# Kernel tuning notes

Measured on AMD Instinct MI355X. Metric: run time of the kernel, lower is better.

Reference implementation:

```python
import jax, jax.numpy as jnp
import numpy as np
import math

D_MODEL, D_INNER, D_STATE, D_CONV, DT_RANK = 768, 1536, 16, 4, 48
BATCH, SEQLEN = 2, 1024
DT_MIN, DT_MAX = 1e-4, 1.0


def setup_inputs() -> dict:
    key = jax.random.key(0)
    ks = jax.random.split(key, 10)
    D, N, R, K = D_INNER, D_STATE, DT_RANK, D_CONV
    total_out = 2 * D + R + 2 * D * N

    def xavier(k, shape):
        fan_in, fan_out = shape[1], shape[0]
        a = math.sqrt(6.0 / (fan_in + fan_out))
        return jax.random.uniform(k, shape, jnp.float32, -a, a)

    x = jax.random.normal(ks[0], (BATCH, SEQLEN, D_MODEL), jnp.float32)
    W_in = xavier(ks[1], (total_out, D_MODEL))
    W_dt = xavier(ks[2], (D, R))
    W_out = xavier(ks[3], (D_MODEL, D))
    W_res = xavier(ks[4], (D, D_MODEL))
    conv_w = jax.random.normal(ks[5], (D, K), jnp.float32) * (1.0 / math.sqrt(K))
    conv_b = jnp.zeros((D,), jnp.float32)
    # A_log init: log(1..N) per inner channel
    A_log = jnp.broadcast_to(jnp.log(jnp.arange(1, N + 1, dtype=jnp.float32)), (D, N))
    Dskip = jnp.ones((D,), jnp.float32)
    # dt_bias = inverse_softplus(exp(uniform in [log dt_min, log dt_max]))
    dt = jnp.exp(jax.random.uniform(ks[6], (D,), jnp.float32) * (math.log(DT_MAX) - math.log(DT_MIN)) + math.log(DT_MIN))
    dt_bias = dt + jnp.log(-jnp.expm1(-dt))
    norm_w = jnp.ones((D,), jnp.float32)
    ln_w = jnp.ones((D_MODEL,), jnp.float32)
    ln_b = jnp.zeros((D_MODEL,), jnp.float32)
    return {
        "x": x, "ln_w": ln_w, "ln_b": ln_b, "W_in": W_in, "W_dt": W_dt,
        "conv_w": conv_w, "conv_b": conv_b, "A_log": A_log, "Dskip": Dskip,
        "dt_bias": dt_bias, "norm_w": norm_w, "W_res": W_res, "W_out": W_out,
    }


def _forward(x, ln_w, ln_b, W_in, W_dt, conv_w, conv_b, A_log, Dskip, dt_bias, norm_w, W_res, W_out):
    B, L, _ = x.shape
    D, N = A_log.shape
    K = conv_w.shape[1]
    R = W_dt.shape[1]
    # pre LayerNorm
    mu = x.mean(-1, keepdims=True)
    var = ((x - mu) ** 2).mean(-1, keepdims=True)
    xn = (x - mu) * jax.lax.rsqrt(var + 1e-5) * ln_w + ln_b
    # fused input projection, then split
    p = jnp.einsum('bld,od->blo', xn, W_in)  # (B,L,2D+R+2DN)
    z = p[..., :D]
    u = p[..., D:2 * D]
    dth = p[..., 2 * D:2 * D + R]
    Bpar = p[..., 2 * D + R:2 * D + R + D * N].reshape(B, L, D, N)
    Cpar = p[..., 2 * D + R + D * N:].reshape(B, L, D, N)
    # causal depthwise conv over time on u
    uc = jax.lax.conv_general_dilated(
        u.transpose(0, 2, 1), conv_w[:, None, :], (1,), [(K - 1, 0)],
        feature_group_count=D, dimension_numbers=('NCH', 'OIH', 'NCH'))
    u = (uc + conv_b[None, :, None]).transpose(0, 2, 1)  # (B,L,D)
    # dt: low-rank proj + bias -> softplus -> clamp
    dt = jnp.clip(jax.nn.softplus(jnp.einsum('blr,dr->bld', dth, W_dt) + dt_bias), DT_MIN, DT_MAX)
    A = -jnp.exp(A_log)  # (D,N), negative
    dA = jnp.exp(dt[..., None] * A)          # (B,L,D,N)
    dBu = (dt * u)[..., None] * Bpar         # (B,L,D,N)

    def step(h, inp):
        dA_t, dBu_t, C_t = inp               # each (B,D,N)
        h = dA_t * h + dBu_t
        return h, (C_t * h).sum(-1)          # y_t: (B,D)

    h0 = jnp.zeros((B, D, N), x.dtype)
    _, ys = jax.lax.scan(step, h0, (dA.transpose(1, 0, 2, 3),
                                    dBu.transpose(1, 0, 2, 3),
                                    Cpar.transpose(1, 0, 2, 3)))
    y = ys.transpose(1, 0, 2) + u * Dskip    # (B,L,D)
    # fused gated RMSNorm + inner residual
    res = jnp.einsum('blm,dm->bld', x, W_res)
    g = y * jax.nn.silu(z)
    g = g * jax.lax.rsqrt((g * g).mean(-1, keepdims=True) + 1e-6) * norm_w + res
    return jnp.einsum('bld,md->blm', g, W_out)


def reference(x, ln_w, ln_b, W_in, W_dt, conv_w, conv_b, A_log, Dskip, dt_bias, norm_w, W_res, W_out):
    return _forward(x, ln_w, ln_b, W_in, W_dt, conv_w, conv_b, A_log, Dskip, dt_bias, norm_w, W_res, W_out)
```

## Files before the change

### kernel.cpp

```cpp
#include <hip/hip_runtime.h>


typedef unsigned short u16;
typedef __bf16 bf16x8 __attribute__((ext_vector_type(8)));
typedef float f32x4 __attribute__((ext_vector_type(4)));

#define OPAD 52480
#define OTOT 52272
#define DI   1536
#define DM   768
#define Z0   0
#define U0   1536
#define DTH0 3072
#define B0   3120
#define C0   27696

#define SCAN_P 64
#define SCAN_T 16
#define SPF    4

__device__ static inline u16 f2bf(float f) {
    unsigned u = __float_as_uint(f);
    u += 0x7fffu + ((u >> 16) & 1u);
    return (u16)(u >> 16);
}
__device__ static inline float bf2f(u16 s) {
    return __uint_as_float(((unsigned)s) << 16);
}

__device__ static inline void gload16(const void* g, void* l) {
    __builtin_amdgcn_global_load_lds(
        (const __attribute__((address_space(1))) unsigned int*)g,
        (__attribute__((address_space(3))) unsigned int*)l, 16, 0, 0);
}

__device__ static inline void unpack8(uint4 v, float* f) {
    unsigned w0 = v.x, w1 = v.y, w2 = v.z, w3 = v.w;
    f[0] = __uint_as_float(w0 << 16); f[1] = __uint_as_float(w0 & 0xffff0000u);
    f[2] = __uint_as_float(w1 << 16); f[3] = __uint_as_float(w1 & 0xffff0000u);
    f[4] = __uint_as_float(w2 << 16); f[5] = __uint_as_float(w2 & 0xffff0000u);
    f[6] = __uint_as_float(w3 << 16); f[7] = __uint_as_float(w3 & 0xffff0000u);
}

__global__ void cvt_kernel(const float* __restrict__ src, u16* __restrict__ dst,
                           long n_src, long n_tot) {
    long i4 = ((long)blockIdx.x * 256 + threadIdx.x) * 4;
    if (i4 >= n_tot) return;
    ushort4 o;
    if (i4 < n_src) {
        float4 v = *(const float4*)(src + i4);
        o.x = f2bf(v.x); o.y = f2bf(v.y); o.z = f2bf(v.z); o.w = f2bf(v.w);
    } else {
        o.x = o.y = o.z = o.w = 0;
    }
    *(ushort4*)(dst + i4) = o;
}

__device__ static inline void block_reduce2(float& a, float& b) {
    #pragma unroll
    for (int o = 32; o > 0; o >>= 1) {
        a += __shfl_down(a, o);
        b += __shfl_down(b, o);
    }
    __shared__ float sa[4], sb[4];
    int lane = threadIdx.x & 63, w = threadIdx.x >> 6;
    if (lane == 0) { sa[w] = a; sb[w] = b; }
    __syncthreads();
    a = sa[0] + sa[1] + sa[2] + sa[3];
    b = sb[0] + sb[1] + sb[2] + sb[3];
}

__global__ void __launch_bounds__(256) ln_kernel(const float* __restrict__ x,
        const float* __restrict__ w, const float* __restrict__ b,
        u16* __restrict__ xnbf, u16* __restrict__ xbf) {
    int m = blockIdx.x, tid = threadIdx.x;
    const float* xr = x + (size_t)m * DM;
    float v[3];
    v[0] = xr[tid]; v[1] = xr[tid + 256]; v[2] = xr[tid + 512];
    float s = v[0] + v[1] + v[2];
    float ss = v[0]*v[0] + v[1]*v[1] + v[2]*v[2];
    block_reduce2(s, ss);
    float mu = s * (1.f / DM);
    float var = ss * (1.f / DM) - mu * mu;
    float inv = rsqrtf(var + 1e-5f);
    #pragma unroll
    for (int i = 0; i < 3; ++i) {
        int d = tid + i * 256;
        float xn = (v[i] - mu) * inv * w[d] + b[d];
        xnbf[(size_t)m * DM + d] = f2bf(xn);
        xbf[(size_t)m * DM + d] = f2bf(v[i]);
    }
}

template <int OUT_BF16>
__global__ void __launch_bounds__(256) gemm_bt(const u16* __restrict__ A,
        const u16* __restrict__ B, void* __restrict__ C, int K, int ldc) {
    __shared__ u16 smem[2 * 128 * 64];
    u16* As = smem;
    u16* Bs = smem + 128 * 64;
    int tid = threadIdx.x;
    int m0 = blockIdx.x * 128, n0 = blockIdx.y * 128;
    int lane = tid & 63, wave = tid >> 6;
    int wm = wave >> 1, wn = wave & 1;
    int l15 = lane & 15, l4 = lane >> 4;
    f32x4 acc[4][4] = {};
    const u16* Ag = A + (size_t)m0 * K;
    const u16* Bg = B + (size_t)n0 * K;
    int crow = tid >> 3;
    int ccol = ((tid & 7) ^ ((tid >> 3) & 7)) * 8;
    int ldsoff = (tid & 192) * 16;
    int xr = l15 & 7;

    for (int k0 = 0; k0 < K; k0 += 64) {
        __syncthreads();
        #pragma unroll
        for (int it = 0; it < 4; ++it) {
            gload16(Ag + (size_t)(it * 32 + crow) * K + k0 + ccol,
                    (char*)As + it * 4096 + ldsoff);
            gload16(Bg + (size_t)(it * 32 + crow) * K + k0 + ccol,
                    (char*)Bs + it * 4096 + ldsoff);
        }
        __syncthreads();
        const u16* Arow = As + (wm * 64 + l15) * 64;
        const u16* Brow = Bs + (wn * 64 + l15) * 64;
        #pragma unroll
        for (int kk8 = 0; kk8 < 8; kk8 += 4) {
            int sw = ((l4 + kk8) ^ xr) * 8;
            bf16x8 af[4], bfr[4];
            #pragma unroll
            for (int i = 0; i < 4; ++i) af[i] = *(const bf16x8*)(Arow + i * 16 * 64 + sw);
            #pragma unroll
            for (int j = 0; j < 4; ++j) bfr[j] = *(const bf16x8*)(Brow + j * 16 * 64 + sw);
            #pragma unroll
            for (int i = 0; i < 4; ++i)
                #pragma unroll
                for (int j = 0; j < 4; ++j)
                    acc[i][j] = __builtin_amdgcn_mfma_f32_16x16x32_bf16(
                        af[i], bfr[j], acc[i][j], 0, 0, 0);
        }
    }
    #pragma unroll
    for (int i = 0; i < 4; ++i) {
        int row = m0 + wm * 64 + i * 16 + l4 * 4;
        #pragma unroll
        for (int j = 0; j < 4; ++j) {
            int col = n0 + wn * 64 + j * 16 + l15;
            #pragma unroll
            for (int r = 0; r < 4; ++r) {
                size_t off = (size_t)(row + r) * ldc + col;
                if (OUT_BF16) ((u16*)C)[off] = f2bf(acc[i][j][r]);
                else          ((float*)C)[off] = acc[i][j][r];
            }
        }
    }
}

#define G2_BUF  65536
#define G2_HALF 16384
#define G2_BOFF 32768

__global__ void __launch_bounds__(512, 2) gemm256_bt(const u16* __restrict__ A,
        const u16* __restrict__ B, u16* __restrict__ C, int K, int ldc) {
    __shared__ u16 smem[65536];
    char* smemc = (char*)smem;
    const int tid = threadIdx.x;
    const int l = tid & 63, w = tid >> 6;
    const int wm = w >> 2, wn = w & 3;
    const int l15 = l & 15, l4 = l >> 4;
    const int flat = blockIdx.y * 8 + blockIdx.x;
    const int wg = (flat & 7) * 205 + (flat >> 3);
    const int m0 = (wg & 7) * 256, n0 = (wg >> 3) * 256;
    const int NT = K >> 6;

    const int rA = l15 >> 1;
    const int rdoff = rA * 128 + ((((l4 << 1) + (l15 & 1)) ^ ((rA & 3) << 1)) << 4);
    const int wpr = (l & 7) ^ (((l >> 3) & 3) << 1);
    const int srow = w * 32 + ((l >> 3) << 1) + (wpr & 1);
    const u16* Ast = A + (size_t)(m0 + srow) * K + (wpr >> 1) * 8;
    const u16* Bst = B + (size_t)(n0 + srow) * K + (wpr >> 1) * 8;
    const int sdst = w * 2048;

    f32x4 acc[8][4] = {};
    bf16x8 bvK[4];

#define G2_STAGE(MATP, MOFF, nxt, sh, tk)                                      \
    gload16(MATP + (size_t)(tk) * 64 + (sh) * 32,                              \
            smemc + (nxt) * G2_BUF + (MOFF) + (sh) * G2_HALF + sdst);          \
    gload16(MATP + (size_t)16 * K + (size_t)(tk) * 64 + (sh) * 32,             \
            smemc + (nxt) * G2_BUF + (MOFF) + (sh) * G2_HALF + sdst + 1024);

#define G2_PHASE(cur, nxt, rh, h, READB, SMAT, SMOFF, sh, tk, DO_VM)           \
    {                                                                          \
        G2_STAGE(SMAT, SMOFF, nxt, sh, tk);                                    \
        const char* Ab = smemc + (cur) * G2_BUF + (h) * G2_HALF                \
                         + (wm * 128 + (rh) * 64) * 64 + rdoff;                \
        bf16x8 af[4];                                                          \
        if (READB) {                                                           \
            const char* Bb = smemc + (cur) * G2_BUF + G2_BOFF + (h) * G2_HALF  \
                             + (wn * 64) * 64 + rdoff;                         \
            _Pragma("unroll")                                                  \
            for (int j = 0; j < 4; ++j)                                        \
                bvK[j] = *(const bf16x8*)(Bb + j * 1024);                      \
        }                                                                      \
        _Pragma("unroll")                                                      \
        for (int i = 0; i < 4; ++i) af[i] = *(const bf16x8*)(Ab + i * 1024);   \
        __builtin_amdgcn_s_barrier();                                          \
        __builtin_amdgcn_s_setprio(1);                                         \
        _Pragma("unroll")                                                      \
        for (int i = 0; i < 4; ++i)                                            \
            _Pragma("unroll")                                                  \
            for (int j = 0; j < 4; ++j)                                        \
                acc[(rh) * 4 + i][j] = __builtin_amdgcn_mfma_f32_16x16x32_bf16(\
                    af[i], bvK[j], acc[(rh) * 4 + i][j], 0, 0, 0);             \
        __builtin_amdgcn_s_setprio(0);                                         \
        if (DO_VM) asm volatile("s_waitcnt vmcnt(4)" ::: "memory");            \
        __builtin_amdgcn_s_barrier();                                          \
    }

#define G2_TILE(cur, nxt, tk)                                                  \
    G2_PHASE(cur, nxt, 0, 0, 1, Ast, 0,       0, tk, 0)                        \
    G2_PHASE(cur, nxt, 1, 0, 0, Bst, G2_BOFF, 0, tk, 1)                        \
    G2_PHASE(cur, nxt, 0, 1, 1, Ast, 0,       1, tk, 0)                        \
    G2_PHASE(cur, nxt, 1, 1, 0, Bst, G2_BOFF, 1, tk, 1)

    G2_STAGE(Ast, 0,       0, 0, 0);
    G2_STAGE(Bst, G2_BOFF, 0, 0, 0);
    G2_STAGE(Ast, 0,       0, 1, 0);
    G2_STAGE(Bst, G2_BOFF, 0, 1, 0);
    asm volatile("s_waitcnt vmcnt(4)" ::: "memory");
    __builtin_amdgcn_s_barrier();

    for (int t = 0; t < NT; t += 2) {
        int tk1 = t + 1;
        int tk2 = (t + 2 < NT) ? t + 2 : NT - 1;
        G2_TILE(0, 1, tk1)
        G2_TILE(1, 0, tk2)
    }

    #pragma unroll
    for (int ai = 0; ai < 8; ++ai) {
        int row = m0 + wm * 128 + ai * 16 + l4 * 4;
        #pragma unroll
        for (int j = 0; j < 4; ++j) {
            int col = n0 + wn * 64 + j * 16 + l15;
            #pragma unroll
            for (int r = 0; r < 4; ++r)
                C[(size_t)(row + r) * ldc + col] = f2bf(acc[ai][j][r]);
        }
    }
#undef G2_STAGE
#undef G2_PHASE
#undef G2_TILE
}

__global__ void __launch_bounds__(256) conv_kernel(const u16* __restrict__ p,
        const float* __restrict__ cw, const float* __restrict__ cb,
        float* __restrict__ u) {
    int d = blockIdx.x * 256 + threadIdx.x;
    int m = blockIdx.y;
    int l = m & 1023;
    int bm = m - l;
    float acc = cb[d];
    #pragma unroll
    for (int j = 0; j < 4; ++j) {
        int ls = l - 3 + j;
        if (ls >= 0)
            acc += cw[d * 4 + j] * bf2f(p[(size_t)(bm + ls) * OPAD + U0 + d]);
    }
    u[(size_t)m * DI + d] = acc;
}

__global__ void __launch_bounds__(256) dt_kernel(const u16* __restrict__ p,
        const float* __restrict__ Wdt, const float* __restrict__ dt_bias,
        float* __restrict__ dt) {
    int m0 = blockIdx.x * 16, tid = threadIdx.x;
    __shared__ float dth_s[16 * 48];
    for (int i = tid; i < 16 * 48; i += 256)
        dth_s[i] = bf2f(p[(size_t)(m0 + i / 48) * OPAD + DTH0 + (i % 48)]);
    __syncthreads();
    #pragma unroll
    for (int ii = 0; ii < 6; ++ii) {
        int d = ii * 256 + tid;
        float base = dt_bias[d];
        float acc[16];
        #pragma unroll
        for (int mm = 0; mm < 16; ++mm) acc[mm] = base;
        for (int r = 0; r < 48; ++r) {
            float wv = Wdt[d * 48 + r];
            #pragma unroll
            for (int mm = 0; mm < 16; ++mm)
                acc[mm] = fmaf(wv, dth_s[mm * 48 + r], acc[mm]);
        }
        #pragma unroll
        for (int mm = 0; mm < 16; ++mm) {
            float xv = acc[mm];
            float sp = xv > 20.f ? xv : log1pf(__expf(xv));
            sp = fminf(fmaxf(sp, 1e-4f), 1.0f);
            dt[(size_t)(m0 + mm) * DI + d] = sp;
        }
    }
}

__global__ void __launch_bounds__(256, 2) scan1_kernel(const u16* __restrict__ p,
        const float* __restrict__ dt, const float* __restrict__ u,
        const float* __restrict__ A_log,
        float* __restrict__ chkA, float* __restrict__ chkB) {
    int d = blockIdx.x * 256 + threadIdx.x;
    int b = blockIdx.y, c = blockIdx.z;
    int t0base = c * SCAN_T;
    float a[16];
    #pragma unroll
    for (int n = 0; n < 16; ++n) a[n] = -__expf(A_log[d * 16 + n]);
    const u16* pB = p + (size_t)(b * 1024 + t0base) * OPAD + B0 + d * 16;
    const float* dtp = dt + (size_t)(b * 1024 + t0base) * DI + d;
    const float* up  = u  + (size_t)(b * 1024 + t0base) * DI + d;
    uint4 Br[SPF][2]; float dtr[SPF], ur[SPF];
    #pragma unroll
    for (int i = 0; i < SPF; ++i) {
        Br[i][0] = *(const uint4*)(pB + (size_t)i * OPAD);
        Br[i][1] = *(const uint4*)(pB + (size_t)i * OPAD + 8);
        dtr[i] = dtp[(size_t)i * DI];
        ur[i]  = up[(size_t)i * DI];
    }
    float h[16], Av[16];
    #pragma unroll
    for (int n = 0; n < 16; ++n) { h[n] = 0.f; Av[n] = 1.f; }
    for (int t0 = 0; t0 < SCAN_T; t0 += SPF) {
        #pragma unroll
        for (int s = 0; s < SPF; ++s) {
            int t = t0 + s;
            uint4 b0 = Br[s][0], b1 = Br[s][1];
            float dtv = dtr[s], uv = ur[s];
            int tl = t + SPF < SCAN_T ? t + SPF : SCAN_T - 1;
            Br[s][0] = *(const uint4*)(pB + (size_t)tl * OPAD);
            Br[s][1] = *(const uint4*)(pB + (size_t)tl * OPAD + 8);
            dtr[s] = dtp[(size_t)tl * DI];
            ur[s]  = up[(size_t)tl * DI];
            float Bf[16];
            unpack8(b0, Bf); unpack8(b1, Bf + 8);
            float dtu = dtv * uv;
            #pragma unroll
            for (int n = 0; n < 16; ++n) {
                float dA = __expf(dtv * a[n]);
                h[n] = fmaf(dA, h[n], dtu * Bf[n]);
                Av[n] *= dA;
            }
        }
    }
    size_t o = (((size_t)c * 2 + b) * 1536 + d) * 16;
    #pragma unroll
    for (int k = 0; k < 4; ++k) {
        *(float4*)(chkA + o + k * 4) = make_float4(Av[4*k], Av[4*k+1], Av[4*k+2], Av[4*k+3]);
        *(float4*)(chkB + o + k * 4) = make_float4(h[4*k], h[4*k+1], h[4*k+2], h[4*k+3]);
    }
}

__global__ void __launch_bounds__(256) scan_comb_kernel(const float* __restrict__ chkA,
        const float* __restrict__ chkB, float* __restrict__ hstart) {
    int idx = blockIdx.x * 256 + threadIdx.x;
    float hs = 0.f;
    for (int c = 0; c < SCAN_P; ++c) {
        size_t o = (size_t)c * 49152 + idx;
        hstart[o] = hs;
        hs = fmaf(chkA[o], hs, chkB[o]);
    }
}

__global__ void __launch_bounds__(256, 2) scan2_kernel(const u16* __restrict__ p,
        const float* __restrict__ dt, const float* __restrict__ u,
        const float* __restrict__ A_log, const float* __restrict__ Dskip,
        const float* __restrict__ hstart, float* __restrict__ y) {
    int d = blockIdx.x * 256 + threadIdx.x;
    int b = blockIdx.y, c = blockIdx.z;
    int t0base = c * SCAN_T;
    float a[16];
    #pragma unroll
    for (int n = 0; n < 16; ++n) a[n] = -__expf(A_log[d * 16 + n]);
    float Dsk = Dskip[d];
    const u16* pB = p + (size_t)(b * 1024 + t0base) * OPAD + B0 + d * 16;
    const u16* pC = p + (size_t)(b * 1024 + t0base) * OPAD + C0 + d * 16;
    const float* dtp = dt + (size_t)(b * 1024 + t0base) * DI + d;
    const float* up  = u  + (size_t)(b * 1024 + t0base) * DI + d;
    float* yp        = y  + (size_t)(b * 1024 + t0base) * DI + d;
    uint4 Br[SPF][2], Cr[SPF][2]; float dtr[SPF], ur[SPF];
    #pragma unroll
    for (int i = 0; i < SPF; ++i) {
        Br[i][0] = *(const uint4*)(pB + (size_t)i * OPAD);
        Br[i][1] = *(const uint4*)(pB + (size_t)i * OPAD + 8);
        Cr[i][0] = *(const uint4*)(pC + (size_t)i * OPAD);
        Cr[i][1] = *(const uint4*)(pC + (size_t)i * OPAD + 8);
        dtr[i] = dtp[(size_t)i * DI];
        ur[i]  = up[(size_t)i * DI];
    }
    float h[16];
    {
        size_t o = ((size_t)c * 3072 + (size_t)b * 1536 + d) * 16;
        #pragma unroll
        for (int k = 0; k < 4; ++k) {
            float4 hv = *(const float4*)(hstart + o + k * 4);
            h[4*k] = hv.x; h[4*k+1] = hv.y; h[4*k+2] = hv.z; h[4*k+3] = hv.w;
        }
    }
    for (int t0 = 0; t0 < SCAN_T; t0 += SPF) {
        #pragma unroll
        for (int s = 0; s < SPF; ++s) {
            int t = t0 + s;
            uint4 b0 = Br[s][0], b1 = Br[s][1], c0 = Cr[s][0], c1 = Cr[s][1];
            float dtv = dtr[s], uv = ur[s];
            int tl = t + SPF < SCAN_T ? t + SPF : SCAN_T - 1;
            Br[s][0] = *(const uint4*)(pB + (size_t)tl * OPAD);
            Br[s][1] = *(const uint4*)(pB + (size_t)tl * OPAD + 8);
            Cr[s][0] = *(const uint4*)(pC + (size_t)tl * OPAD);
            Cr[s][1] = *(const uint4*)(pC + (size_t)tl * OPAD + 8);
            dtr[s] = dtp[(size_t)tl * DI];
            ur[s]  = up[(size_t)tl * DI];
            float Bf[16], Cf[16];
            unpack8(b0, Bf); unpack8(b1, Bf + 8);
            unpack8(c0, Cf); unpack8(c1, Cf + 8);
            float dtu = dtv * uv;
            #pragma unroll
            for (int n = 0; n < 16; ++n) {
                float dA = __expf(dtv * a[n]);
                h[n] = fmaf(dA, h[n], dtu * Bf[n]);
            }
            float a0 = fmaf(Cf[0], h[0], uv * Dsk), a1 = Cf[1] * h[1];
            float a2 = Cf[2] * h[2], a3 = Cf[3] * h[3];
            #pragma unroll
            for (int n = 4; n < 16; n += 4) {
                a0 = fmaf(Cf[n],   h[n],   a0);
                a1 = fmaf(Cf[n+1], h[n+1], a1);
                a2 = fmaf(Cf[n+2], h[n+2], a2);
                a3 = fmaf(Cf[n+3], h[n+3], a3);
            }
            yp[(size_t)t * DI] = (a0 + a1) + (a2 + a3);
        }
    }
}

__global__ void __launch_bounds__(256) gate_kernel(const u16* __restrict__ p,
        const float* __restrict__ y, const float* __restrict__ res,
        const float* __restrict__ norm_w, u16* __restrict__ g) {
    int m = blockIdx.x, tid = threadIdx.x;
    const u16* pz = p + (size_t)m * OPAD + Z0;
    const float* yr = y + (size_t)m * DI;
    float gp[6];
    float ss = 0.f, dummy = 0.f;
    #pragma unroll
    for (int i = 0; i < 6; ++i) {
        int d = i * 256 + tid;
        float z = bf2f(pz[d]);
        float gv = yr[d] * z / (1.f + __expf(-z));
        gp[i] = gv;
        ss += gv * gv;
    }
    block_reduce2(ss, dummy);
    float scale = rsqrtf(ss * (1.f / DI) + 1e-6f);
    #pragma unroll
    for (int i = 0; i < 6; ++i) {
        int d = i * 256 + tid;
        float val = gp[i] * scale * norm_w[d] + res[(size_t)m * DI + d];
        g[(size_t)m * DI + d] = f2bf(val);
    }
}

extern "C" void kernel_launch(void* const* d_in, const int* in_sizes, int n_in,
                              void* d_out, int out_size, void* d_ws, size_t ws_size,
                              hipStream_t stream) {
    const float* x       = (const float*)d_in[0];
    const float* ln_w    = (const float*)d_in[1];
    const float* ln_b    = (const float*)d_in[2];
    const float* W_in    = (const float*)d_in[3];
    const float* W_dt    = (const float*)d_in[4];
    const float* conv_w  = (const float*)d_in[5];
    const float* conv_b  = (const float*)d_in[6];
    const float* A_log   = (const float*)d_in[7];
    const float* Dskip   = (const float*)d_in[8];
    const float* dt_bias = (const float*)d_in[9];
    const float* norm_w  = (const float*)d_in[10];
    const float* W_res   = (const float*)d_in[11];
    const float* W_out   = (const float*)d_in[12];
    float* out = (float*)d_out;

    char* wsb = (char*)d_ws;
    u16* Wbf     = (u16*)(wsb + 0);
    u16* Wresbf  = (u16*)(wsb + 80609280);
    u16* Woutbf  = (u16*)(wsb + 82968576);
    u16* xnbf    = (u16*)(wsb + 85327872);
    u16* xbf     = (u16*)(wsb + 88473600);
    u16* pbuf    = (u16*)(wsb + 91619328);
    float* ucv   = (float*)(wsb + 306577408);
    float* dtv   = (float*)(wsb + 319160320);
    float* ybuf  = (float*)(wsb + 331743232);
    float* resb  = (float*)(wsb + 344326144);
    u16* gbuf    = (u16*)(wsb + 356909056);
    float* chkA  = (float*)(wsb + 0);
    float* chkB  = (float*)(wsb + 12582912);
    float* hst   = (float*)(wsb + 25165824);

    cvt_kernel<<<39360, 256, 0, stream>>>(W_in, Wbf, (long)OTOT * DM, (long)OPAD * DM);
    cvt_kernel<<<1152, 256, 0, stream>>>(W_res, Wresbf, (long)DI * DM, (long)DI * DM);
    cvt_kernel<<<1152, 256, 0, stream>>>(W_out, Woutbf, (long)DM * DI, (long)DM * DI);
    ln_kernel<<<2048, 256, 0, stream>>>(x, ln_w, ln_b, xnbf, xbf);
    gemm256_bt<<<dim3(8, 205), 512, 0, stream>>>(xnbf, Wbf, pbuf, DM, OPAD);
    gemm_bt<0><<<dim3(16, 12), 256, 0, stream>>>(xbf, Wresbf, resb, DM, DI);
    conv_kernel<<<dim3(6, 2048), 256, 0, stream>>>(pbuf, conv_w, conv_b, ucv);
    dt_kernel<<<128, 256, 0, stream>>>(pbuf, W_dt, dt_bias, dtv);
    scan1_kernel<<<dim3(6, 2, SCAN_P), 256, 0, stream>>>(pbuf, dtv, ucv, A_log, chkA, chkB);
    scan_comb_kernel<<<192, 256, 0, stream>>>(chkA, chkB, hst);
    scan2_kernel<<<dim3(6, 2, SCAN_P), 256, 0, stream>>>(pbuf, dtv, ucv, A_log, Dskip, hst, ybuf);
    gate_kernel<<<2048, 256, 0, stream>>>(pbuf, ybuf, resb, norm_w, gbuf);
    gemm_bt<0><<<dim3(16, 6), 256, 0, stream>>>(gbuf, Woutbf, out, DI, DM);
}
```

Measured before the change: 705.4 us.

## Fuse W_in bf16 conversion into GEMM loads and conv into scan kernels

The big input-projection GEMM now streams the fp32 W_in directly into an LDS scratch area, converts it to bf16 in-kernel (zeroing padded rows), and writes it into the B tile. This removes the separate cvt pass over the ~40M-element weight and its bf16 write and re-read. The depthwise causal conv is also folded into both scan kernels via a rolling 3-value window, which removes the conv kernel and the fp32 u buffer round trip. The cost is double the B-operand global traffic in fp32, extra LDS and more waitcnt/barrier steps in the GEMM pipeline, and duplicated conv arithmetic in scan1 and scan2.

After: 893.8 us. 26.7% more time.

```diff
diff --git a/kernel.cpp b/kernel.cpp
--- a/kernel.cpp
+++ b/kernel.cpp
@@ -26,6 +26,9 @@
 }
 __device__ static inline float bf2f(u16 s) {
     return __uint_as_float(((unsigned)s) << 16);
+}
+__device__ static inline unsigned pack2(float lo, float hi) {
+    return (unsigned)f2bf(lo) | ((unsigned)f2bf(hi) << 16);
 }
 
 __device__ static inline void gload16(const void* g, void* l) {
@@ -158,10 +161,11 @@
 #define G2_BUF  65536
 #define G2_HALF 16384
 #define G2_BOFF 32768
+#define G2_SCR  131072
 
 __global__ void __launch_bounds__(512, 2) gemm256_bt(const u16* __restrict__ A,
-        const u16* __restrict__ B, u16* __restrict__ C, int K, int ldc) {
-    __shared__ u16 smem[65536];
+        const float* __restrict__ B, u16* __restrict__ C, int K, int ldc) {
+    __shared__ u16 smem[81920];
     char* smemc = (char*)smem;
     const int tid = threadIdx.x;
     const int l = tid & 63, w = tid >> 6;
@@ -177,65 +181,94 @@
     const int wpr = (l & 7) ^ (((l >> 3) & 3) << 1);
     const int srow = w * 32 + ((l >> 3) << 1) + (wpr & 1);
     const u16* Ast = A + (size_t)(m0 + srow) * K + (wpr >> 1) * 8;
-    const u16* Bst = B + (size_t)(n0 + srow) * K + (wpr >> 1) * 8;
+    const int nrow0 = n0 + srow, nrow1 = nrow0 + 16;
+    const int oobA = nrow0 >= OTOT, oobB = nrow1 >= OTOT;
+    const float* Bf0 = B + (size_t)(oobA ? 0 : nrow0) * K + (wpr >> 1) * 8;
+    const float* Bf1 = B + (size_t)(oobB ? 0 : nrow1) * K + (wpr >> 1) * 8;
     const int sdst = w * 2048;
 
     f32x4 acc[8][4] = {};
     bf16x8 bvK[4];
 
-#define G2_STAGE(MATP, MOFF, nxt, sh, tk)                                      \
-    gload16(MATP + (size_t)(tk) * 64 + (sh) * 32,                              \
-            smemc + (nxt) * G2_BUF + (MOFF) + (sh) * G2_HALF + sdst);          \
-    gload16(MATP + (size_t)16 * K + (size_t)(tk) * 64 + (sh) * 32,             \
-            smemc + (nxt) * G2_BUF + (MOFF) + (sh) * G2_HALF + sdst + 1024);
-
-#define G2_PHASE(cur, nxt, rh, h, READB, SMAT, SMOFF, sh, tk, DO_VM)           \
+#define G2_ASTAGE(nxt, sh, tk)                                                 \
+    gload16(Ast + (size_t)(tk) * 64 + (sh) * 32,                               \
+            smemc + (nxt) * G2_BUF + (sh) * G2_HALF + sdst);                   \
+    gload16(Ast + (size_t)16 * K + (size_t)(tk) * 64 + (sh) * 32,              \
+            smemc + (nxt) * G2_BUF + (sh) * G2_HALF + sdst + 1024);
+
+#define G2_BISSUE(QS, qh, qc, tk)                                              \
+    {   const float* bq = ((qc) ? Bf1 : Bf0) + (size_t)(tk) * 64 + (qh) * 32;  \
+        gload16(bq,     smemc + G2_SCR + (QS) * 16384 + sdst);                 \
+        gload16(bq + 4, smemc + G2_SCR + (QS) * 16384 + sdst + 1024); }
+
+#define G2_BCVT(QS, wbuf, wh, wc)                                              \
+    {   const char* scr = smemc + G2_SCR + (QS) * 16384 + sdst + l * 16;       \
+        f32x4 flo = *(const f32x4*)scr;                                        \
+        f32x4 fhi = *(const f32x4*)(scr + 1024);                               \
+        uint4 ov;                                                              \
+        ov.x = pack2(flo[0], flo[1]); ov.y = pack2(flo[2], flo[3]);            \
+        ov.z = pack2(fhi[0], fhi[1]); ov.w = pack2(fhi[2], fhi[3]);            \
+        if ((wc) ? oobB : oobA) ov = make_uint4(0, 0, 0, 0);                   \
+        *(uint4*)(smemc + (wbuf) * G2_BUF + G2_BOFF + (wh) * G2_HALF           \
+                  + sdst + (wc) * 1024 + l * 16) = ov; }
+
+#define G2_PH(cur, nxt, rh, h, ASTG, QS, qh, qc, tk, DOW, wbuf, wh, wc, VN)    \
     {                                                                          \
-        G2_STAGE(SMAT, SMOFF, nxt, sh, tk);                                    \
+        asm volatile("s_waitcnt vmcnt(" #VN ")" ::: "memory");                 \
+        if (DOW) { G2_BCVT(QS, wbuf, wh, wc) }                                 \
+        if (ASTG) { G2_ASTAGE(nxt, h, tk) }                                    \
+        G2_BISSUE(QS, qh, qc, tk)                                              \
         const char* Ab = smemc + (cur) * G2_BUF + (h) * G2_HALF                \
                          + (wm * 128 + (rh) * 64) * 64 + rdoff;                \
         bf16x8 af[4];                                                          \
-        if (READB) {                                                           \
+        if (!(rh)) {                                                           \
             const char* Bb = smemc + (cur) * G2_BUF + G2_BOFF + (h) * G2_HALF  \
                              + (wn * 64) * 64 + rdoff;                         \
-            _Pragma("unroll")                                                  \
-            for (int j = 0; j < 4; ++j)                                        \
+            _Pragma("unroll") for (int j = 0; j < 4; ++j)                      \
                 bvK[j] = *(const bf16x8*)(Bb + j * 1024);                      \
         }                                                                      \
-        _Pragma("unroll")                                                      \
-        for (int i = 0; i < 4; ++i) af[i] = *(const bf16x8*)(Ab + i * 1024);   \
+        _Pragma("unroll") for (int i = 0; i < 4; ++i)                          \
+            af[i] = *(const bf16x8*)(Ab + i * 1024);                           \
+        asm volatile("s_waitcnt lgkmcnt(0)" ::: "memory");                     \
         __builtin_amdgcn_s_barrier();                                          \
         __builtin_amdgcn_s_setprio(1);                                         \
-        _Pragma("unroll")                                                      \
-        for (int i = 0; i < 4; ++i)                                            \
-            _Pragma("unroll")                                                  \
-            for (int j = 0; j < 4; ++j)                                        \
+        _Pragma("unroll") for (int i = 0; i < 4; ++i)                          \
+            _Pragma("unroll") for (int j = 0; j < 4; ++j)                      \
                 acc[(rh) * 4 + i][j] = __builtin_amdgcn_mfma_f32_16x16x32_bf16(\
                     af[i], bvK[j], acc[(rh) * 4 + i][j], 0, 0, 0);             \
         __builtin_amdgcn_s_setprio(0);                                         \
-        if (DO_VM) asm volatile("s_waitcnt vmcnt(4)" ::: "memory");            \
         __builtin_amdgcn_s_barrier();                                          \
     }
 
-#define G2_TILE(cur, nxt, tk)                                                  \
-    G2_PHASE(cur, nxt, 0, 0, 1, Ast, 0,       0, tk, 0)                        \
-    G2_PHASE(cur, nxt, 1, 0, 0, Bst, G2_BOFF, 0, tk, 1)                        \
-    G2_PHASE(cur, nxt, 0, 1, 1, Ast, 0,       1, tk, 0)                        \
-    G2_PHASE(cur, nxt, 1, 1, 0, Bst, G2_BOFF, 1, tk, 1)
-
-    G2_STAGE(Ast, 0,       0, 0, 0);
-    G2_STAGE(Bst, G2_BOFF, 0, 0, 0);
-    G2_STAGE(Ast, 0,       0, 1, 0);
-    G2_STAGE(Bst, G2_BOFF, 0, 1, 0);
-    asm volatile("s_waitcnt vmcnt(4)" ::: "memory");
+#define G2_TILE(cur, nxt, tk, W01)                                             \
+    G2_PH(cur, nxt, 0, 0, 1, 0, 0, 0, tk, W01, cur, 1, 0, 2)                   \
+    G2_PH(cur, nxt, 1, 0, 0, 1, 0, 1, tk, W01, cur, 1, 1, 4)                   \
+    G2_PH(cur, nxt, 0, 1, 1, 0, 1, 0, tk, 1,   nxt, 0, 0, 2)                   \
+    G2_PH(cur, nxt, 1, 1, 0, 1, 1, 1, tk, 1,   nxt, 0, 1, 4)
+
+    G2_ASTAGE(0, 0, 0);
+    G2_ASTAGE(0, 1, 0);
+    G2_BISSUE(0, 0, 0, 0)
+    G2_BISSUE(1, 0, 1, 0)
+    asm volatile("s_waitcnt vmcnt(2)" ::: "memory");
+    G2_BCVT(0, 0, 0, 0)
+    G2_BISSUE(0, 1, 0, 0)
+    asm volatile("s_waitcnt vmcnt(2)" ::: "memory");
+    G2_BCVT(1, 0, 0, 1)
+    G2_BISSUE(1, 1, 1, 0)
+    asm volatile("s_waitcnt vmcnt(2)" ::: "memory");
+    G2_BCVT(0, 0, 1, 0)
+    asm volatile("s_waitcnt vmcnt(0)" ::: "memory");
+    G2_BCVT(1, 0, 1, 1)
+    asm volatile("s_waitcnt lgkmcnt(0)" ::: "memory");
     __builtin_amdgcn_s_barrier();
 
-    for (int t = 0; t < NT; t += 2) {
-        int tk1 = t + 1;
-        int tk2 = (t + 2 < NT) ? t + 2 : NT - 1;
-        G2_TILE(0, 1, tk1)
-        G2_TILE(1, 0, tk2)
-    }
+    G2_TILE(0, 1, 1, 0)
+    for (int t = 1; t + 1 < NT; t += 2) {
+        G2_TILE(1, 0, t + 1, 1)
+        G2_TILE(0, 1, (t + 2 < NT ? t + 2 : NT - 1), 1)
+    }
+    G2_TILE(1, 0, NT - 1, 1)
 
     #pragma unroll
     for (int ai = 0; ai < 8; ++ai) {
@@ -248,26 +281,11 @@
                 C[(size_t)(row + r) * ldc + col] = f2bf(acc[ai][j][r]);
         }
     }
-#undef G2_STAGE
-#undef G2_PHASE
+#undef G2_ASTAGE
+#undef G2_BISSUE
+#undef G2_BCVT
+#undef G2_PH
 #undef G2_TILE
-}
-
-__global__ void __launch_bounds__(256) conv_kernel(const u16* __restrict__ p,
-        const float* __restrict__ cw, const float* __restrict__ cb,
-        float* __restrict__ u) {
-    int d = blockIdx.x * 256 + threadIdx.x;
-    int m = blockIdx.y;
-    int l = m & 1023;
-    int bm = m - l;
-    float acc = cb[d];
-    #pragma unroll
-    for (int j = 0; j < 4; ++j) {
-        int ls = l - 3 + j;
-        if (ls >= 0)
-            acc += cw[d * 4 + j] * bf2f(p[(size_t)(bm + ls) * OPAD + U0 + d]);
-    }
-    u[(size_t)m * DI + d] = acc;
 }
 
 __global__ void __launch_bounds__(256) dt_kernel(const u16* __restrict__ p,
@@ -302,8 +320,8 @@
 }
 
 __global__ void __launch_bounds__(256, 2) scan1_kernel(const u16* __restrict__ p,
-        const float* __restrict__ dt, const float* __restrict__ u,
-        const float* __restrict__ A_log,
+        const float* __restrict__ dt, const float* __restrict__ A_log,
+        const float* __restrict__ cw, const float* __restrict__ cb,
         float* __restrict__ chkA, float* __restrict__ chkB) {
     int d = blockIdx.x * 256 + threadIdx.x;
     int b = blockIdx.y, c = blockIdx.z;
@@ -311,16 +329,25 @@
     float a[16];
     #pragma unroll
     for (int n = 0; n < 16; ++n) a[n] = -__expf(A_log[d * 16 + n]);
+    float cw0 = cw[d*4], cw1 = cw[d*4+1], cw2 = cw[d*4+2], cw3 = cw[d*4+3];
+    float cbv = cb[d];
     const u16* pB = p + (size_t)(b * 1024 + t0base) * OPAD + B0 + d * 16;
+    const u16* pU = p + (size_t)(b * 1024 + t0base) * OPAD + U0 + d;
     const float* dtp = dt + (size_t)(b * 1024 + t0base) * DI + d;
-    const float* up  = u  + (size_t)(b * 1024 + t0base) * DI + d;
-    uint4 Br[SPF][2]; float dtr[SPF], ur[SPF];
+    float x1, x2, x3;
+    if (c == 0) { x1 = x2 = x3 = 0.f; }
+    else {
+        x1 = bf2f(*(pU - (long)OPAD));
+        x2 = bf2f(*(pU - 2L * OPAD));
+        x3 = bf2f(*(pU - 3L * OPAD));
+    }
+    uint4 Br[SPF][2]; float dtr[SPF], xur[SPF];
     #pragma unroll
     for (int i = 0; i < SPF; ++i) {
         Br[i][0] = *(const uint4*)(pB + (size_t)i * OPAD);
         Br[i][1] = *(const uint4*)(pB + (size_t)i * OPAD + 8);
         dtr[i] = dtp[(size_t)i * DI];
-        ur[i]  = up[(size_t)i * DI];
+        xur[i] = bf2f(pU[(size_t)i * OPAD]);
     }
     float h[16], Av[16];
     #pragma unroll
@@ -330,12 +357,18 @@
         for (int s = 0; s < SPF; ++s) {
             int t = t0 + s;
             uint4 b0 = Br[s][0], b1 = Br[s][1];
-            float dtv = dtr[s], uv = ur[s];
+            float dtv = dtr[s], xt = xur[s];
             int tl = t + SPF < SCAN_T ? t + SPF : SCAN_T - 1;
             Br[s][0] = *(const uint4*)(pB + (size_t)tl * OPAD);
             Br[s][1] = *(const uint4*)(pB + (size_t)tl * OPAD + 8);
             dtr[s] = dtp[(size_t)tl * DI];
-            ur[s]  = up[(size_t)tl * DI];
+            xur[s] = bf2f(pU[(size_t)tl * OPAD]);
+            float uv = cbv;
+            uv = fmaf(cw0, x3, uv);
+            uv = fmaf(cw1, x2, uv);
+            uv = fmaf(cw2, x1, uv);
+            uv = fmaf(cw3, xt, uv);
+            x3 = x2; x2 = x1; x1 = xt;
             float Bf[16];
             unpack8(b0, Bf); unpack8(b1, Bf + 8);
             float dtu = dtv * uv;
@@ -367,8 +400,9 @@
 }
 
 __global__ void __launch_bounds__(256, 2) scan2_kernel(const u16* __restrict__ p,
-        const float* __restrict__ dt, const float* __restrict__ u,
-        const float* __restrict__ A_log, const float* __restrict__ Dskip,
+        const float* __restrict__ dt, const float* __restrict__ A_log,
+        const float* __restrict__ cw, const float* __restrict__ cb,
+        const float* __restrict__ Dskip,
         const float* __restrict__ hstart, float* __restrict__ y) {
     int d = blockIdx.x * 256 + threadIdx.x;
     int b = blockIdx.y, c = blockIdx.z;
@@ -377,12 +411,21 @@
     #pragma unroll
     for (int n = 0; n < 16; ++n) a[n] = -__expf(A_log[d * 16 + n]);
     float Dsk = Dskip[d];
+    float cw0 = cw[d*4], cw1 = cw[d*4+1], cw2 = cw[d*4+2], cw3 = cw[d*4+3];
+    float cbv = cb[d];
     const u16* pB = p + (size_t)(b * 1024 + t0base) * OPAD + B0 + d * 16;
     const u16* pC = p + (size_t)(b * 1024 + t0base) * OPAD + C0 + d * 16;
+    const u16* pU = p + (size_t)(b * 1024 + t0base) * OPAD + U0 + d;
     const float* dtp = dt + (size_t)(b * 1024 + t0base) * DI + d;
-    const float* up  = u  + (size_t)(b * 1024 + t0base) * DI + d;
     float* yp        = y  + (size_t)(b * 1024 + t0base) * DI + d;
-    uint4 Br[SPF][2], Cr[SPF][2]; float dtr[SPF], ur[SPF];
+    float x1, x2, x3;
+    if (c == 0) { x1 = x2 = x3 = 0.f; }
+    else {
+        x1 = bf2f(*(pU - (long)OPAD));
+        x2 = bf2f(*(pU - 2L * OPAD));
+        x3 = bf2f(*(pU - 3L * OPAD));
+    }
+    uint4 Br[SPF][2], Cr[SPF][2]; float dtr[SPF], xur[SPF];
     #pragma unroll
     for (int i = 0; i < SPF; ++i) {
         Br[i][0] = *(const uint4*)(pB + (size_t)i * OPAD);
@@ -390,7 +433,7 @@
         Cr[i][0] = *(const uint4*)(pC + (size_t)i * OPAD);
         Cr[i][1] = *(const uint4*)(pC + (size_t)i * OPAD + 8);
         dtr[i] = dtp[(size_t)i * DI];
-        ur[i]  = up[(size_t)i * DI];
+        xur[i] = bf2f(pU[(size_t)i * OPAD]);
     }
     float h[16];
     {
@@ -406,14 +449,20 @@
         for (int s = 0; s < SPF; ++s) {
             int t = t0 + s;
             uint4 b0 = Br[s][0], b1 = Br[s][1], c0 = Cr[s][0], c1 = Cr[s][1];
-            float dtv = dtr[s], uv = ur[s];
+            float dtv = dtr[s], xt = xur[s];
             int tl = t + SPF < SCAN_T ? t + SPF : SCAN_T - 1;
             Br[s][0] = *(const uint4*)(pB + (size_t)tl * OPAD);
             Br[s][1] = *(const uint4*)(pB + (size_t)tl * OPAD + 8);
             Cr[s][0] = *(const uint4*)(pC + (size_t)tl * OPAD);
             Cr[s][1] = *(const uint4*)(pC + (size_t)tl * OPAD + 8);
             dtr[s] = dtp[(size_t)tl * DI];
-            ur[s]  = up[(size_t)tl * DI];
+            xur[s] = bf2f(pU[(size_t)tl * OPAD]);
+            float uv = cbv;
+            uv = fmaf(cw0, x3, uv);
+            uv = fmaf(cw1, x2, uv);
+            uv = fmaf(cw2, x1, uv);
+            uv = fmaf(cw3, xt, uv);
+            x3 = x2; x2 = x1; x1 = xt;
             float Bf[16], Cf[16];
             unpack8(b0, Bf); unpack8(b1, Bf + 8);
             unpack8(c0, Cf); unpack8(c1, Cf + 8);
@@ -482,13 +531,11 @@
     float* out = (float*)d_out;
 
     char* wsb = (char*)d_ws;
-    u16* Wbf     = (u16*)(wsb + 0);
     u16* Wresbf  = (u16*)(wsb + 80609280);
     u16* Woutbf  = (u16*)(wsb + 82968576);
     u16* xnbf    = (u16*)(wsb + 85327872);
     u16* xbf     = (u16*)(wsb + 88473600);
     u16* pbuf    = (u16*)(wsb + 91619328);
-    float* ucv   = (float*)(wsb + 306577408);
     float* dtv   = (float*)(wsb + 319160320);
     float* ybuf  = (float*)(wsb + 331743232);
     float* resb  = (float*)(wsb + 344326144);
@@ -497,17 +544,15 @@
     float* chkB  = (float*)(wsb + 12582912);
     float* hst   = (float*)(wsb + 25165824);
 
-    cvt_kernel<<<39360, 256, 0, stream>>>(W_in, Wbf, (long)OTOT * DM, (long)OPAD * DM);
     cvt_kernel<<<1152, 256, 0, stream>>>(W_res, Wresbf, (long)DI * DM, (long)DI * DM);
     cvt_kernel<<<1152, 256, 0, stream>>>(W_out, Woutbf, (long)DM * DI, (long)DM * DI);
     ln_kernel<<<2048, 256, 0, stream>>>(x, ln_w, ln_b, xnbf, xbf);
-    gemm256_bt<<<dim3(8, 205), 512, 0, stream>>>(xnbf, Wbf, pbuf, DM, OPAD);
+    gemm256_bt<<<dim3(8, 205), 512, 0, stream>>>(xnbf, W_in, pbuf, DM, OPAD);
     gemm_bt<0><<<dim3(16, 12), 256, 0, stream>>>(xbf, Wresbf, resb, DM, DI);
-    conv_kernel<<<dim3(6, 2048), 256, 0, stream>>>(pbuf, conv_w, conv_b, ucv);
     dt_kernel<<<128, 256, 0, stream>>>(pbuf, W_dt, dt_bias, dtv);
-    scan1_kernel<<<dim3(6, 2, SCAN_P), 256, 0, stream>>>(pbuf, dtv, ucv, A_log, chkA, chkB);
+    scan1_kernel<<<dim3(6, 2, SCAN_P), 256, 0, stream>>>(pbuf, dtv, A_log, conv_w, conv_b, chkA, chkB);
     scan_comb_kernel<<<192, 256, 0, stream>>>(chkA, chkB, hst);
-    scan2_kernel<<<dim3(6, 2, SCAN_P), 256, 0, stream>>>(pbuf, dtv, ucv, A_log, Dskip, hst, ybuf);
+    scan2_kernel<<<dim3(6, 2, SCAN_P), 256, 0, stream>>>(pbuf, dtv, A_log, conv_w, conv_b, Dskip, hst, ybuf);
     gate_kernel<<<2048, 256, 0, stream>>>(pbuf, ybuf, resb, norm_w, gbuf);
     gemm_bt<0><<<dim3(16, 6), 256, 0, stream>>>(gbuf, Woutbf, out, DI, DM);
 }
```
